# Kernel optimization log

Measured on AMD Instinct MI355X. Metric: run time of the kernel, lower is better.

Reference implementation:

```python
import jax, jax.numpy as jnp
import numpy as np

# Static configuration matching init_kwargs
LR_SHAPES = ((64, 64), (128, 128), (256, 256))
H0, W0 = LR_SHAPES[0]          # selected layer (layer_number = 0)
UP = (8, 8)                     # upscale factors -> output_dim = 64
OUT_DIM = UP[0] * UP[1]
KERNEL = (3, 3)
PAD = (1, 1)
BATCH = 64
WEIGHTS_IN = 189                # 9 + 36 + 144


def _unfold(x, kernel, stride, pad):
    """torch.F.unfold equivalent for NCHW input with C==1.
    x: (N, 1, H, W) -> (N, kh*kw, L) with row-major spatial positions."""
    patches = jax.lax.conv_general_dilated_patches(
        x,
        filter_shape=kernel,
        window_strides=stride,
        padding=((pad[0], pad[0]), (pad[1], pad[1])),
        dimension_numbers=('NCHW', 'OIHW', 'NCHW'),
    )  # (N, kh*kw, H_out, W_out)
    n, k, h, w = patches.shape
    return patches.reshape(n, k, h * w)


def setup_inputs() -> dict:
    key = jax.random.key(0)
    k0, k1, k2, kw = jax.random.split(key, 4)
    x0 = jax.random.normal(k0, (BATCH, 1, 64, 64), dtype=jnp.float32)
    x1 = jax.random.normal(k1, (BATCH, 1, 128, 128), dtype=jnp.float32)
    x2 = jax.random.normal(k2, (BATCH, 1, 256, 256), dtype=jnp.float32)
    # original uses uniform(-stdv, stdv) with tiny stdv; small-scale normal keeps
    # the softmax non-degenerate while matching the magnitude regime
    weight = jax.random.normal(kw, (WEIGHTS_IN, OUT_DIM), dtype=jnp.float32) * 0.01
    return {"x0": x0, "x1": x1, "x2": x2, "weight": weight}


def reference(x0, x1, x2, weight):
    xs = (x0, x1, x2)
    cols = []
    for j, (hj, wj) in enumerate(LR_SHAPES):
        s = (hj // H0, wj // W0)                       # scale vs selected layer
        f = (KERNEL[0] * s[0], KERNEL[1] * s[1])       # scaled kernel
        p = (PAD[0] * s[0], PAD[1] * s[1])             # scaled padding
        cols.append(_unfold(xs[j], f, s, p))           # (N, 9*s0*s1, L)
    X = jnp.concatenate(cols, axis=1)                  # (N, 189, L), L = H0*W0

    # per-pixel attention weights: matmul + ReLU + softmax
    logits = jax.nn.relu(jnp.einsum('nkl,ko->nlo', X, weight))  # (N, L, 64)
    soft = jax.nn.softmax(logits, axis=-1)                       # (N, L, 64)

    # reassemble: each LR pixel value scaled by its 64 attention weights (C==1)
    xsel = x0.reshape(x0.shape[0], H0 * W0)            # (N, L)
    out = xsel[:, :, None] * soft                      # (N, L, 64)

    # fold(kernel=1) == reshape to (N, 64, H0, W0)
    n = out.shape[0]
    out = out.transpose(0, 2, 1).reshape(n, OUT_DIM, H0, W0)

    # pixel shuffle -> (N, 1, H0*up0, W0*up1)
    out = out.reshape(n, 1, UP[0], UP[1], H0, W0)
    out = out.transpose(0, 1, 4, 2, 5, 3)
    return out.reshape(n, 1, H0 * UP[0], W0 * UP[1])
```

## Files before the change

### kernel.cpp

```cpp
#include <hip/hip_runtime.h>

typedef _Float16 f16;
typedef f16 f16x8 __attribute__((ext_vector_type(8)));
typedef f16 f16x4 __attribute__((ext_vector_type(4)));
typedef float f32x4 __attribute__((ext_vector_type(4)));

#define S0 28
#define S1 48
#define S2 92
#define T0OFF 0
#define T1OFF (11 * S0)
#define T2OFF (T1OFF + 20 * S1)
#define TILEH (T2OFF + 40 * S2)
#define LOG2E 1.4426950408889634f

__global__ void prep_wt(const float* __restrict__ W, f16* __restrict__ Wt) {
  const int f = blockIdx.x * 256 + threadIdx.x;
  const int s = f >> 8;
  const int t = (f >> 6) & 3;
  const int lane = f & 63;
  const int quad = lane >> 4, ln = lane & 15;
  const int n = t * 16 + ln;
  f16 vals[8];
  #pragma unroll
  for (int j = 0; j < 8; ++j) {
    int kp = s * 32 + quad * 8 + j;
    int orig = -1;
    if (kp < 16)      { int ki = kp >> 2, kj = kp & 3;                   if (ki < 3 && kj < 3) orig = 3*ki + kj; }
    else if (kp < 64) { int kk = kp - 16; int ki = kk >> 3, kj = kk & 7;  if (kj < 6)          orig = 9 + 6*ki + kj; }
    else              { int kk = kp - 64; int ki = kk >> 4, kj = kk & 15; if (kj < 12)         orig = 45 + 12*ki + kj; }
    vals[j] = (f16)((orig >= 0) ? W[orig * 64 + n] : 0.f);
  }
  *(f16x8*)(Wt + (size_t)f * 8) = *(const f16x8*)vals;
}

__global__ __launch_bounds__(256, 6) void fuse_kernel(
    const float* __restrict__ x0, const float* __restrict__ x1,
    const float* __restrict__ x2, const f16* __restrict__ Wt,
    float* __restrict__ out)
{
  __shared__ __align__(16) f16 tiles[TILEH];

  const int tid  = threadIdx.x;
  const int bid  = ((blockIdx.x & 7) << 8) | (blockIdx.x >> 3);
  const int nb   = bid >> 5;
  const int ty   = (bid >> 2) & 7;
  const int tx   = bid & 3;
  const int lane = tid & 63;
  const int wid  = tid >> 6;
  const int ln   = lane & 15;
  const int quad = lane >> 4;

  const f16* __restrict__ wfrag = Wt + (size_t)lane * 8;

  f32x4 v2[4];
  {
    const float* img = x2 + nb * 65536;
    #pragma unroll
    for (int i = 0; i < 4; ++i) {
      int idx = tid + 256 * i;
      int r  = idx / 22, c4 = idx - r * 22;
      int gy = ty * 32 - 4 + r;
      int gx = tx * 64 - 8 + 4 * c4;
      bool inb = (i < 3 || tid < 112) && ((unsigned)gy < 256u) && ((unsigned)gx < 256u);
      v2[i] = inb ? *(const f32x4*)(img + gy * 256 + gx) : (f32x4){0.f, 0.f, 0.f, 0.f};
    }
  }

  {
    const float* img = x1 + nb * 16384;
    int idx = tid;
    int r  = idx / 11, c4 = idx - r * 11;
    int gy = ty * 16 - 2 + r;
    int gx = tx * 32 - 4 + 4 * c4;
    bool inb = (idx < 220) && ((unsigned)gy < 128u) && ((unsigned)gx < 128u);
    f32x4 t = inb ? *(const f32x4*)(img + gy * 128 + gx) : (f32x4){0.f, 0.f, 0.f, 0.f};
    if (idx < 220) {
      f16x4 h; h[0] = (f16)t[0]; h[1] = (f16)t[1]; h[2] = (f16)t[2]; h[3] = (f16)t[3];
      *(f16x4*)&tiles[T1OFF + r * S1 + 4 * c4] = h;
    }
  }
  {
    const float* img = x0 + nb * 4096;
    int idx = tid;
    int r  = idx / 6, c4 = idx - r * 6;
    int gy = ty * 8 - 1 + r;
    int gx = tx * 16 - 4 + 4 * c4;
    bool inb = (idx < 66) && ((unsigned)gy < 64u) && ((unsigned)gx < 64u);
    f32x4 t = inb ? *(const f32x4*)(img + gy * 64 + gx) : (f32x4){0.f, 0.f, 0.f, 0.f};
    if (idx < 66) {
      f16x4 h; h[0] = (f16)t[0]; h[1] = (f16)t[1]; h[2] = (f16)t[2]; h[3] = (f16)t[3];
      *(f16x4*)&tiles[T0OFF + r * S0 + 4 * c4] = h;
    }
  }

  float xs[2];
  #pragma unroll
  for (int cc = 0; cc < 2; ++cc)
    xs[cc] = x0[nb * 4096 + (ty * 8 + wid * 2 + cc) * 64 + tx * 16 + ln];

  #pragma unroll
  for (int i = 0; i < 4; ++i) {
    if (i < 3 || tid < 112) {
      int idx = tid + 256 * i;
      int r  = idx / 22, c4 = idx - r * 22;
      f16x4 h; h[0] = (f16)v2[i][0]; h[1] = (f16)v2[i][1];
      h[2] = (f16)v2[i][2]; h[3] = (f16)v2[i][3];
      *(f16x4*)&tiles[T2OFF + r * S2 + 4 * c4] = h;
    }
  }

  f16x8 bf0[4];
  #pragma unroll
  for (int t = 0; t < 4; ++t)
    bf0[t] = *(const f16x8*)(wfrag + t * 512);

  __syncthreads();

  f32x4 acc[2][4];
  #pragma unroll
  for (int c = 0; c < 2; ++c)
    #pragma unroll
    for (int t = 0; t < 4; ++t)
      acc[c][t] = (f32x4){0.f, 0.f, 0.f, 0.f};

  {
    #pragma unroll
    for (int cc = 0; cc < 2; ++cc) {
      const int py = wid * 2 + cc;
      f16x8 a;
      if (quad < 2) {
        const int a0 = T0OFF + (py + 2 * quad) * S0 + ln + 3;
        #pragma unroll
        for (int j = 0; j < 4; ++j) a[j]     = tiles[a0 + j];
        #pragma unroll
        for (int j = 0; j < 4; ++j) a[4 + j] = tiles[a0 + S0 + j];
      } else {
        const int a1 = T1OFF + (2 * py + quad - 2) * S1 + 2 * ln + 2;
        #pragma unroll
        for (int j = 0; j < 8; ++j) a[j] = tiles[a1 + j];
      }
      #pragma unroll
      for (int t = 0; t < 4; ++t)
        acc[cc][t] = __builtin_amdgcn_mfma_f32_16x16x32_f16(bf0[t], a, acc[cc][t], 0, 0, 0);
    }
  }
  {
    f16x8 bf[4];
    #pragma unroll
    for (int t = 0; t < 4; ++t)
      bf[t] = *(const f16x8*)(wfrag + (4 + t) * 512);
    #pragma unroll
    for (int cc = 0; cc < 2; ++cc) {
      const int py = wid * 2 + cc;
      const int a1 = T1OFF + (2 * py + 2 + quad) * S1 + 2 * ln + 2;
      f16x8 a;
      #pragma unroll
      for (int j = 0; j < 8; ++j) a[j] = tiles[a1 + j];
      #pragma unroll
      for (int t = 0; t < 4; ++t)
        acc[cc][t] = __builtin_amdgcn_mfma_f32_16x16x32_f16(bf[t], a, acc[cc][t], 0, 0, 0);
    }
  }
  #pragma unroll 3
  for (int s = 2; s < 8; ++s) {
    f16x8 bf[4];
    #pragma unroll
    for (int t = 0; t < 4; ++t)
      bf[t] = *(const f16x8*)(wfrag + (s * 4 + t) * 512);
    #pragma unroll
    for (int cc = 0; cc < 2; ++cc) {
      const int py = wid * 2 + cc;
      const int b2 = T2OFF + (4 * py + 2 * (s - 2) + (quad >> 1)) * S2 + 4 * ln + 4 + 8 * (quad & 1);
      f16x4 lo = *(const f16x4*)&tiles[b2];
      f16x4 hi = *(const f16x4*)&tiles[b2 + 4];
      f16x8 a;
      a[0] = lo[0]; a[1] = lo[1]; a[2] = lo[2]; a[3] = lo[3];
      a[4] = hi[0]; a[5] = hi[1]; a[6] = hi[2]; a[7] = hi[3];
      #pragma unroll
      for (int t = 0; t < 4; ++t)
        acc[cc][t] = __builtin_amdgcn_mfma_f32_16x16x32_f16(bf[t], a, acc[cc][t], 0, 0, 0);
    }
  }

  const int gx8 = (tx * 16 + ln) * 8;
  #pragma unroll
  for (int cc = 0; cc < 2; ++cc) {
    float v[4][4];
    float m = 0.f;
    #pragma unroll
    for (int t = 0; t < 4; ++t)
      #pragma unroll
      for (int r = 0; r < 4; ++r) {
        float x = fmaxf(acc[cc][t][r], 0.f);
        v[t][r] = x;
        m = fmaxf(m, x);
      }
    m = fmaxf(m, __shfl_xor(m, 16));
    m = fmaxf(m, __shfl_xor(m, 32));

    float sden = 0.f;
    #pragma unroll
    for (int t = 0; t < 4; ++t)
      #pragma unroll
      for (int r = 0; r < 4; ++r) {
        float e = exp2f((v[t][r] - m) * LOG2E);
        v[t][r] = e;
        sden += e;
      }
    sden += __shfl_xor(sden, 16);
    sden += __shfl_xor(sden, 32);

    const float sc = xs[cc] * __builtin_amdgcn_rcpf(sden);
    const int gy = ty * 8 + wid * 2 + cc;
    float* op = out + nb * 262144 + (gy * 8 + (quad >> 1)) * 512 + gx8 + 4 * (quad & 1);
    #pragma unroll
    for (int t = 0; t < 4; ++t) {
      f32x4 w;
      w[0] = v[t][0] * sc; w[1] = v[t][1] * sc;
      w[2] = v[t][2] * sc; w[3] = v[t][3] * sc;
      *(f32x4*)(op + t * 1024) = w;
    }
  }
}

extern "C" void kernel_launch(void* const* d_in, const int* in_sizes, int n_in,
                              void* d_out, int out_size, void* d_ws, size_t ws_size,
                              hipStream_t stream) {
  const float* x0 = (const float*)d_in[0];
  const float* x1 = (const float*)d_in[1];
  const float* x2 = (const float*)d_in[2];
  const float* W  = (const float*)d_in[3];
  float* outp     = (float*)d_out;
  f16* Wt         = (f16*)d_ws;

  prep_wt<<<dim3(8), dim3(256), 0, stream>>>(W, Wt);
  fuse_kernel<<<dim3(2048), dim3(256), 0, stream>>>(x0, x1, x2, Wt, outp);
}
```

Measured before the change: 106.9 us.

## Give each wave a private LDS halo tile and drop the block barrier

Result: no change. 108.8 us (median of 2 runs) (+1.8%).

```diff
diff --git a/kernel.cpp b/kernel.cpp
--- a/kernel.cpp
+++ b/kernel.cpp
@@ -5,13 +5,10 @@
 typedef f16 f16x4 __attribute__((ext_vector_type(4)));
 typedef float f32x4 __attribute__((ext_vector_type(4)));
 
-#define S0 28
-#define S1 48
-#define S2 92
-#define T0OFF 0
-#define T1OFF (11 * S0)
-#define T2OFF (T1OFF + 20 * S1)
-#define TILEH (T2OFF + 40 * S2)
+#define X0OFF 0
+#define X1OFF 140
+#define X2OFF 524
+#define WSL   2048
 #define LOG2E 1.4426950408889634f
 
 __global__ void prep_wt(const float* __restrict__ W, f16* __restrict__ Wt) {
@@ -39,74 +36,79 @@
     const float* __restrict__ x2, const f16* __restrict__ Wt,
     float* __restrict__ out)
 {
-  __shared__ __align__(16) f16 tiles[TILEH];
+  __shared__ __align__(16) f16 tiles[4 * WSL];
 
   const int tid  = threadIdx.x;
   const int bid  = ((blockIdx.x & 7) << 8) | (blockIdx.x >> 3);
   const int nb   = bid >> 5;
-  const int ty   = (bid >> 2) & 7;
+  const int ty8  = (bid >> 2) & 7;
   const int tx   = bid & 3;
   const int lane = tid & 63;
   const int wid  = tid >> 6;
   const int ln   = lane & 15;
   const int quad = lane >> 4;
 
+  f16* sl = tiles + wid * WSL;
   const f16* __restrict__ wfrag = Wt + (size_t)lane * 8;
 
-  f32x4 v2[4];
+  f32x4 v2[6];
   {
     const float* img = x2 + nb * 65536;
     #pragma unroll
-    for (int i = 0; i < 4; ++i) {
-      int idx = tid + 256 * i;
-      int r  = idx / 22, c4 = idx - r * 22;
-      int gy = ty * 32 - 4 + r;
+    for (int i = 0; i < 6; ++i) {
+      int idx = lane + 64 * i;
+      int rr = idx / 22, c4 = idx - rr * 22;
+      int gy = ty8 * 32 - 4 + 8 * wid + rr;
       int gx = tx * 64 - 8 + 4 * c4;
-      bool inb = (i < 3 || tid < 112) && ((unsigned)gy < 256u) && ((unsigned)gx < 256u);
+      bool inb = (i < 5 || lane < 32) && ((unsigned)gy < 256u) && ((unsigned)gx < 256u);
       v2[i] = inb ? *(const f32x4*)(img + gy * 256 + gx) : (f32x4){0.f, 0.f, 0.f, 0.f};
     }
   }
 
   {
     const float* img = x1 + nb * 16384;
-    int idx = tid;
-    int r  = idx / 11, c4 = idx - r * 11;
-    int gy = ty * 16 - 2 + r;
-    int gx = tx * 32 - 4 + 4 * c4;
-    bool inb = (idx < 220) && ((unsigned)gy < 128u) && ((unsigned)gx < 128u);
-    f32x4 t = inb ? *(const f32x4*)(img + gy * 128 + gx) : (f32x4){0.f, 0.f, 0.f, 0.f};
-    if (idx < 220) {
+    #pragma unroll
+    for (int i = 0; i < 2; ++i) {
+      int idx = lane + 64 * i;
+      int rr = idx / 11, c4 = idx - rr * 11;
+      int gy = ty8 * 16 - 2 + 4 * wid + rr;
+      int gx = tx * 32 - 4 + 4 * c4;
+      bool ok  = (i < 1 || lane < 24);
+      bool inb = ok && ((unsigned)gy < 128u) && ((unsigned)gx < 128u);
+      f32x4 t = inb ? *(const f32x4*)(img + gy * 128 + gx) : (f32x4){0.f, 0.f, 0.f, 0.f};
+      if (ok) {
+        f16x4 h; h[0] = (f16)t[0]; h[1] = (f16)t[1]; h[2] = (f16)t[2]; h[3] = (f16)t[3];
+        *(f16x4*)&sl[X1OFF + rr * 48 + 4 * c4] = h;
+      }
+    }
+  }
+  {
+    const float* img = x0 + nb * 4096;
+    int rr = lane / 6, c4 = lane - rr * 6;
+    int gy = ty8 * 8 - 1 + 2 * wid + rr;
+    int gx = tx * 16 - 4 + 4 * c4;
+    bool ok  = lane < 30;
+    bool inb = ok && ((unsigned)gy < 64u) && ((unsigned)gx < 64u);
+    f32x4 t = inb ? *(const f32x4*)(img + gy * 64 + gx) : (f32x4){0.f, 0.f, 0.f, 0.f};
+    if (ok) {
       f16x4 h; h[0] = (f16)t[0]; h[1] = (f16)t[1]; h[2] = (f16)t[2]; h[3] = (f16)t[3];
-      *(f16x4*)&tiles[T1OFF + r * S1 + 4 * c4] = h;
-    }
-  }
-  {
-    const float* img = x0 + nb * 4096;
-    int idx = tid;
-    int r  = idx / 6, c4 = idx - r * 6;
-    int gy = ty * 8 - 1 + r;
-    int gx = tx * 16 - 4 + 4 * c4;
-    bool inb = (idx < 66) && ((unsigned)gy < 64u) && ((unsigned)gx < 64u);
-    f32x4 t = inb ? *(const f32x4*)(img + gy * 64 + gx) : (f32x4){0.f, 0.f, 0.f, 0.f};
-    if (idx < 66) {
-      f16x4 h; h[0] = (f16)t[0]; h[1] = (f16)t[1]; h[2] = (f16)t[2]; h[3] = (f16)t[3];
-      *(f16x4*)&tiles[T0OFF + r * S0 + 4 * c4] = h;
+      *(f16x4*)&sl[X0OFF + rr * 28 + 4 * c4] = h;
     }
   }
 
   float xs[2];
   #pragma unroll
   for (int cc = 0; cc < 2; ++cc)
-    xs[cc] = x0[nb * 4096 + (ty * 8 + wid * 2 + cc) * 64 + tx * 16 + ln];
-
-  #pragma unroll
-  for (int i = 0; i < 4; ++i) {
-    if (i < 3 || tid < 112) {
-      int idx = tid + 256 * i;
-      int r  = idx / 22, c4 = idx - r * 22;
+    xs[cc] = x0[nb * 4096 + (ty8 * 8 + 2 * wid + cc) * 64 + tx * 16 + ln];
+
+  #pragma unroll
+  for (int i = 0; i < 6; ++i) {
+    if (i < 5 || lane < 32) {
+      int idx = lane + 64 * i;
+      int rr = idx / 22, c4 = idx - rr * 22;
       f16x4 h; h[0] = (f16)v2[i][0]; h[1] = (f16)v2[i][1];
       h[2] = (f16)v2[i][2]; h[3] = (f16)v2[i][3];
-      *(f16x4*)&tiles[T2OFF + r * S2 + 4 * c4] = h;
+      *(f16x4*)&sl[X2OFF + rr * 92 + 4 * c4] = h;
     }
   }
 
@@ -115,7 +117,6 @@
   for (int t = 0; t < 4; ++t)
     bf0[t] = *(const f16x8*)(wfrag + t * 512);
 
-  __syncthreads();
 
   f32x4 acc[2][4];
   #pragma unroll
@@ -127,18 +128,17 @@
   {
     #pragma unroll
     for (int cc = 0; cc < 2; ++cc) {
-      const int py = wid * 2 + cc;
       f16x8 a;
       if (quad < 2) {
-        const int a0 = T0OFF + (py + 2 * quad) * S0 + ln + 3;
+        const int a0 = X0OFF + (cc + 2 * quad) * 28 + ln + 3;
         #pragma unroll
-        for (int j = 0; j < 4; ++j) a[j]     = tiles[a0 + j];
+        for (int j = 0; j < 4; ++j) a[j]     = sl[a0 + j];
         #pragma unroll
-        for (int j = 0; j < 4; ++j) a[4 + j] = tiles[a0 + S0 + j];
+        for (int j = 0; j < 4; ++j) a[4 + j] = sl[a0 + 28 + j];
       } else {
-        const int a1 = T1OFF + (2 * py + quad - 2) * S1 + 2 * ln + 2;
+        const int a1 = X1OFF + (2 * cc + quad - 2) * 48 + 2 * ln + 2;
         #pragma unroll
-        for (int j = 0; j < 8; ++j) a[j] = tiles[a1 + j];
+        for (int j = 0; j < 8; ++j) a[j] = sl[a1 + j];
       }
       #pragma unroll
       for (int t = 0; t < 4; ++t)
@@ -152,11 +152,10 @@
       bf[t] = *(const f16x8*)(wfrag + (4 + t) * 512);
     #pragma unroll
     for (int cc = 0; cc < 2; ++cc) {
-      const int py = wid * 2 + cc;
-      const int a1 = T1OFF + (2 * py + 2 + quad) * S1 + 2 * ln + 2;
+      const int a1 = X1OFF + (2 * cc + 2 + quad) * 48 + 2 * ln + 2;
       f16x8 a;
       #pragma unroll
-      for (int j = 0; j < 8; ++j) a[j] = tiles[a1 + j];
+      for (int j = 0; j < 8; ++j) a[j] = sl[a1 + j];
       #pragma unroll
       for (int t = 0; t < 4; ++t)
         acc[cc][t] = __builtin_amdgcn_mfma_f32_16x16x32_f16(bf[t], a, acc[cc][t], 0, 0, 0);
@@ -170,10 +169,9 @@
       bf[t] = *(const f16x8*)(wfrag + (s * 4 + t) * 512);
     #pragma unroll
     for (int cc = 0; cc < 2; ++cc) {
-      const int py = wid * 2 + cc;
-      const int b2 = T2OFF + (4 * py + 2 * (s - 2) + (quad >> 1)) * S2 + 4 * ln + 4 + 8 * (quad & 1);
-      f16x4 lo = *(const f16x4*)&tiles[b2];
-      f16x4 hi = *(const f16x4*)&tiles[b2 + 4];
+      const int b2 = X2OFF + (4 * cc + 2 * (s - 2) + (quad >> 1)) * 92 + 4 * ln + 4 + 8 * (quad & 1);
+      f16x4 lo = *(const f16x4*)&sl[b2];
+      f16x4 hi = *(const f16x4*)&sl[b2 + 4];
       f16x8 a;
       a[0] = lo[0]; a[1] = lo[1]; a[2] = lo[2]; a[3] = lo[3];
       a[4] = hi[0]; a[5] = hi[1]; a[6] = hi[2]; a[7] = hi[3];
@@ -212,7 +210,7 @@
     sden += __shfl_xor(sden, 32);
 
     const float sc = xs[cc] * __builtin_amdgcn_rcpf(sden);
-    const int gy = ty * 8 + wid * 2 + cc;
+    const int gy = ty8 * 8 + 2 * wid + cc;
     float* op = out + nb * 262144 + (gy * 8 + (quad >> 1)) * 512 + gx8 + 4 * (quad & 1);
     #pragma unroll
     for (int t = 0; t < 4; ++t) {
```
